# Performance work log

Hardware: AMD Instinct MI355X
Metric: run time of the kernel (lower is better)

## Reference

```python
import jax, jax.numpy as jnp
import numpy as np

B = 256
M = (32, 32, 32)          # size_in modes
N = (32, 32, 32)          # size_out modes
R = (1, 16, 16, 1)        # TT ranks
CORE_SCALE = 0.05


def setup_inputs() -> dict:
    key = jax.random.key(0)
    kx, k0, k1, k2, kb = jax.random.split(key, 5)
    x = jax.random.normal(kx, (B,) + M, dtype=jnp.float32)
    # TT cores: core_i has shape [r_i, n_i, m_i, r_{i+1}]
    core0 = jax.random.normal(k0, (R[0], N[0], M[0], R[1]), dtype=jnp.float32) * CORE_SCALE
    core1 = jax.random.normal(k1, (R[1], N[1], M[1], R[2]), dtype=jnp.float32) * CORE_SCALE
    core2 = jax.random.normal(k2, (R[2], N[2], M[2], R[3]), dtype=jnp.float32) * CORE_SCALE
    bias = jax.random.normal(kb, N, dtype=jnp.float32) * 0.01
    return {"x": x, "core0": core0, "core1": core1, "core2": core2, "bias": bias}


def _tt_matvec(x, cores):
    # y[..., n1..nd] = sum_{m1..md} prod_i core_i[r_i, n_i, m_i, r_{i+1}] * x[..., m1..md]
    d = len(cores)
    batch_shape = x.shape[:-d]
    # z: [B, r, P, m_i, m_{i+1}, ..., m_d]  (P = flattened already-produced n dims)
    z = x.reshape((-1, 1, 1) + x.shape[-d:])
    n_dims = []
    for core in cores:
        r, n, m, s = core.shape
        # contract current input mode m and left rank r; append output mode n
        z = jnp.einsum('rnms,brpm...->bspn...', core, z)
        n_dims.append(n)
        sh = z.shape
        z = z.reshape(sh[:2] + (sh[2] * sh[3],) + sh[4:])  # merge P and n
    return z.reshape(batch_shape + tuple(n_dims))


def reference(x, core0, core1, core2, bias):
    y = _tt_matvec(x, (core0, core1, core2))
    return y + bias
```

## Files before the change

### kernel.cpp

```cpp
#include <hip/hip_runtime.h>


typedef __attribute__((ext_vector_type(8))) short bf16x8;
typedef __attribute__((ext_vector_type(4))) float f32x4;

#define WS_A1   0
#define WS_A0T  262144
#define WS_W2T  278528
#define WS_XT   294912
#define WS_XT_ELEMS 8388608
#define WS_NEED_BYTES ((size_t)(WS_XT + WS_XT_ELEMS) * 2)

__device__ __forceinline__ unsigned short f2bf(float f) {
    union { float f; unsigned int u; } v; v.f = f;
    unsigned int u = v.u;
    u += 0x7fffu + ((u >> 16) & 1u);
    return (unsigned short)(u >> 16);
}

template<bool XT>
__global__ void tt_prep(const float* __restrict__ x,
                        const float* __restrict__ core0,
                        const float* __restrict__ core1,
                        const float* __restrict__ core2,
                        unsigned short* __restrict__ ws)
{
    const int t = threadIdx.x;
    if (XT && blockIdx.x < 8192) {
        __shared__ float tile[32 * 36];
        const int b  = blockIdx.x >> 5;
        const int m2 = blockIdx.x & 31;
        {
            const int m1 = t >> 3, c4 = (t & 7) * 4;
            float4 v = *(const float4*)(x + (size_t)b * 32768 + m1 * 1024 + m2 * 32 + c4);
            *(float4*)&tile[m1 * 36 + c4] = v;
        }
        __syncthreads();
        {
            const int m3 = t >> 3, g = t & 7;
            unsigned short o[4];
            #pragma unroll
            for (int j = 0; j < 4; ++j)
                o[j] = f2bf(tile[(g * 4 + j) * 36 + m3]);
            unsigned short* dst = ws + WS_XT + (size_t)b * 32768 + (m2 * 32 + m3) * 32 + g * 4;
            *(uint2*)dst = *(uint2*)o;
        }
        return;
    }
    const int u = (blockIdx.x - (XT ? 8192 : 0)) * 256 + t;
    unsigned short* A1  = ws + WS_A1;
    unsigned short* A0T = ws + WS_A0T;
    unsigned short* W2T = ws + WS_W2T;
    bf16x8 o;
    if (u < 32768) {
        int e = u * 8;
        int row = e >> 9, col0 = e & 511;
        int n2 = row >> 4, s = row & 15;
        int m2 = col0 >> 4, r0 = col0 & 15;
        const float* src = core1 + n2 * 512 + m2 * 16 + s;
        #pragma unroll
        for (int j = 0; j < 8; ++j) o[j] = (short)f2bf(src[(r0 + j) * 16384]);
        *(bf16x8*)(A1 + e) = o;
    } else if (u < 34816) {
        int e = (u - 32768) * 8;
        int row = e >> 5, m1b = e & 31;
        int n1 = row >> 4, s = row & 15;
        const float* src = core0 + n1 * 512 + m1b * 16 + s;
        #pragma unroll
        for (int j = 0; j < 8; ++j) o[j] = (short)f2bf(src[j * 16]);
        *(bf16x8*)(A0T + e) = o;
    } else if (u < 36864) {
        int e = (u - 34816) * 8;
        int n3 = e >> 9, k20 = e & 511;
        int m3 = k20 >> 4, s0 = k20 & 15;
        const float* src = core2 + n3 * 32 + m3;
        #pragma unroll
        for (int j = 0; j < 8; ++j) o[j] = (short)f2bf(src[(s0 + j) * 1024]);
        *(bf16x8*)(W2T + e) = o;
    }
}

template<bool XT>
__global__ __launch_bounds__(512, 2)
void tt_mfma(const float* __restrict__ x,
             const unsigned short* __restrict__ ws,
             const float* __restrict__ bias,
             float* __restrict__ out)
{
    extern __shared__ char smem[];

    const unsigned short* A1  = ws + WS_A1;
    const unsigned short* A0T = ws + WS_A0T;
    const unsigned short* W2T = ws + WS_W2T;
    const unsigned short* xT  = ws + WS_XT;

    const int t   = threadIdx.x;
    const int l   = t & 63;
    const int w   = t >> 6;
    const int l15 = l & 15;
    const int lg  = l >> 4;

    const int swzid = (blockIdx.x & 7) * 256 + (blockIdx.x >> 3);
    const int bq = swzid >> 5;
    const int n1 = swzid & 31;

    const int swz5 = ((l15 >> 1) & 1) << 5;

    {
        const int lb = w >> 1, ph = w & 1;
        const int b  = bq * 4 + lb;
        char* zb = smem + lb * 32768;
        bf16x8 afrag = *(const bf16x8*)(A0T + n1 * 512 + l15 * 32 + lg * 8);
        if (XT) {
            const unsigned short* xb = xT + (size_t)b * 32768 + lg * 8;
            bf16x8 bfrag[2];
            bfrag[0] = *(const bf16x8*)(xb + (ph * 512 + l15) * 32);
            #pragma unroll
            for (int pti = 0; pti < 32; ++pti) {
                if (pti < 31) {
                    int pn = ph * 512 + (pti + 1) * 16 + l15;
                    bfrag[(pti + 1) & 1] = *(const bf16x8*)(xb + pn * 32);
                }
                int p = ph * 512 + pti * 16 + l15;
                f32x4 c = __builtin_amdgcn_mfma_f32_16x16x32_bf16(
                    afrag, bfrag[pti & 1], (f32x4){0.f, 0.f, 0.f, 0.f}, 0, 0, 0);
                int m2 = p >> 5, m3 = p & 31;
                unsigned short h[4];
                #pragma unroll
                for (int i = 0; i < 4; ++i) h[i] = f2bf(c[i]);
                int off = ((m2 >> 1) << 11) + (m3 << 6) +
                          ((((m2 & 1) << 5) + (lg << 3)) ^ (((m3 >> 1) & 1) << 5));
                *(uint2*)(zb + off) = *(uint2*)h;
            }
        } else {
            const float* xb = x + (size_t)b * 32768 + (lg * 8) * 1024;
            for (int pti = 0; pti < 32; ++pti) {
                int p = ph * 512 + pti * 16 + l15;
                bf16x8 bfrag;
                #pragma unroll
                for (int j = 0; j < 8; ++j) bfrag[j] = (short)f2bf(xb[j * 1024 + p]);
                f32x4 c = __builtin_amdgcn_mfma_f32_16x16x32_bf16(
                    afrag, bfrag, (f32x4){0.f, 0.f, 0.f, 0.f}, 0, 0, 0);
                int m2 = p >> 5, m3 = p & 31;
                unsigned short h[4];
                #pragma unroll
                for (int i = 0; i < 4; ++i) h[i] = f2bf(c[i]);
                int off = ((m2 >> 1) << 11) + (m3 << 6) +
                          ((((m2 & 1) << 5) + (lg << 3)) ^ (((m3 >> 1) & 1) << 5));
                *(uint2*)(zb + off) = *(uint2*)h;
            }
        }
    }
    __syncthreads();

    f32x4 acc[4][8];
    #pragma unroll
    for (int mt = 0; mt < 4; ++mt)
        #pragma unroll
        for (int nt = 0; nt < 8; ++nt)
            acc[mt][nt] = (f32x4){0.f, 0.f, 0.f, 0.f};
    {
        const unsigned short* a1p = A1 + (w * 64 + l15) * 512 + lg * 8;
        const int kofs = (lg << 4) ^ swz5;
        const int rlo = (l15 << 6) + kofs;
        const int rhi = rlo + 1024;

        bf16x8 af[2][4], bf[2][8];
        #pragma unroll
        for (int mt = 0; mt < 4; ++mt)
            af[0][mt] = *(const bf16x8*)(a1p + mt * 8192);
        #pragma unroll
        for (int b4 = 0; b4 < 4; ++b4) {
            char* zb = smem + b4 * 32768;
            bf[0][b4 * 2 + 0] = *(const bf16x8*)(zb + rlo);
            bf[0][b4 * 2 + 1] = *(const bf16x8*)(zb + rhi);
        }
        #pragma unroll
        for (int ks = 0; ks < 16; ++ks) {
            const int cur = ks & 1, nxt = cur ^ 1;
            if (ks < 15) {
                #pragma unroll
                for (int mt = 0; mt < 4; ++mt)
                    af[nxt][mt] = *(const bf16x8*)(a1p + mt * 8192 + (ks + 1) * 32);
                #pragma unroll
                for (int b4 = 0; b4 < 4; ++b4) {
                    char* zb = smem + b4 * 32768 + (ks + 1) * 2048;
                    bf[nxt][b4 * 2 + 0] = *(const bf16x8*)(zb + rlo);
                    bf[nxt][b4 * 2 + 1] = *(const bf16x8*)(zb + rhi);
                }
            }
            __builtin_amdgcn_s_setprio(1);
            #pragma unroll
            for (int mt = 0; mt < 4; ++mt)
                #pragma unroll
                for (int nt = 0; nt < 8; ++nt)
                    acc[mt][nt] = __builtin_amdgcn_mfma_f32_16x16x32_bf16(
                        af[cur][mt], bf[cur][nt], acc[mt][nt], 0, 0, 0);
            __builtin_amdgcn_s_setprio(0);
        }
    }
    __syncthreads();

    {
        #pragma unroll
        for (int mt = 0; mt < 4; ++mt) {
            int n2 = w * 4 + mt;
            int nsw = ((n2 >> 1) & 1) << 5;
            #pragma unroll
            for (int nt = 0; nt < 8; ++nt) {
                char* zb = smem + (nt >> 1) * 32768;
                int m3 = (nt & 1) * 16 + l15;
                unsigned short h[4];
                #pragma unroll
                for (int i = 0; i < 4; ++i) h[i] = f2bf(acc[mt][nt][i]);
                int off = ((m3 >> 1) << 11) + (n2 << 6) +
                          ((((m3 & 1) << 5) + (lg << 3)) ^ nsw);
                *(uint2*)(zb + off) = *(uint2*)h;
            }
        }
    }
    __syncthreads();

    {
        const int lb = w >> 1, n3h = w & 1;
        const int b  = bq * 4 + lb;
        char* zb = smem + lb * 32768;
        f32x4 c[2];
        c[0] = (f32x4){0.f, 0.f, 0.f, 0.f};
        c[1] = (f32x4){0.f, 0.f, 0.f, 0.f};
        const unsigned short* w2p = W2T + (n3h * 16 + l15) * 512 + lg * 8;
        const int kofs = (lg << 4) ^ swz5;
        bf16x8 bfg[2];
        bfg[0] = *(const bf16x8*)(w2p);
        #pragma unroll
        for (int ks = 0; ks < 16; ++ks) {
            if (ks < 15) bfg[(ks + 1) & 1] = *(const bf16x8*)(w2p + (ks + 1) * 32);
            #pragma unroll
            for (int mt = 0; mt < 2; ++mt) {
                int n2 = mt * 16 + l15;
                bf16x8 af = *(const bf16x8*)(zb + ks * 2048 + (n2 << 6) + kofs);
                c[mt] = __builtin_amdgcn_mfma_f32_16x16x32_bf16(af, bfg[ks & 1], c[mt], 0, 0, 0);
            }
        }
        int n3 = n3h * 16 + l15;
        size_t ob = (size_t)b * 32768 + (size_t)n1 * 1024;
        const float* bp2 = bias + n1 * 1024;
        #pragma unroll
        for (int mt = 0; mt < 2; ++mt)
            #pragma unroll
            for (int i = 0; i < 4; ++i) {
                int n2 = mt * 16 + lg * 4 + i;
                out[ob + n2 * 32 + n3] = c[mt][i] + bp2[n2 * 32 + n3];
            }
    }
}

extern "C" void kernel_launch(void* const* d_in, const int* in_sizes, int n_in,
                              void* d_out, int out_size, void* d_ws, size_t ws_size,
                              hipStream_t stream) {
    (void)in_sizes; (void)n_in; (void)out_size;
    const float* x     = (const float*)d_in[0];
    const float* core0 = (const float*)d_in[1];
    const float* core1 = (const float*)d_in[2];
    const float* core2 = (const float*)d_in[3];
    const float* bias  = (const float*)d_in[4];
    float* out = (float*)d_out;
    unsigned short* ws = (unsigned short*)d_ws;

    const int lds_bytes = 4 * 32768;
    if (ws_size >= WS_NEED_BYTES) {
        hipFuncSetAttribute((const void*)tt_mfma<true>,
                            hipFuncAttributeMaxDynamicSharedMemorySize, lds_bytes);
        tt_prep<true><<<8336, 256, 0, stream>>>(x, core0, core1, core2, ws);
        tt_mfma<true><<<2048, 512, lds_bytes, stream>>>(x, ws, bias, out);
    } else {
        hipFuncSetAttribute((const void*)tt_mfma<false>,
                            hipFuncAttributeMaxDynamicSharedMemorySize, lds_bytes);
        tt_prep<false><<<144, 256, 0, stream>>>(x, core0, core1, core2, ws);
        tt_mfma<false><<<2048, 512, lds_bytes, stream>>>(x, ws, bias, out);
    }
}
```

Measured before the change: 229.1 us.

## Halve batches per block to cut LDS and registers for higher occupancy

Each block now handles 2 batch elements instead of 4. That halves LDS use to 64 KB and halves the stage-2 accumulator tile, and the launch bounds now request 4 blocks per CU, with twice as many blocks launched. The explicit double-buffered register prefetch of A1 and the LDS fragments is dropped in favour of per-iteration loads with partial unrolling. The aim is to hide latency through occupancy rather than software pipelining. The trade-off is that each A1 fragment loaded from global memory is reused across fewer batches, so global traffic for A1 rises.

```diff
diff --git a/kernel.cpp b/kernel.cpp
--- a/kernel.cpp
+++ b/kernel.cpp
@@ -81,7 +81,7 @@
 }
 
 template<bool XT>
-__global__ __launch_bounds__(512, 2)
+__global__ __launch_bounds__(512, 4)
 void tt_mfma(const float* __restrict__ x,
              const unsigned short* __restrict__ ws,
              const float* __restrict__ bias,
@@ -100,28 +100,28 @@
     const int l15 = l & 15;
     const int lg  = l >> 4;
 
-    const int swzid = (blockIdx.x & 7) * 256 + (blockIdx.x >> 3);
+    const int swzid = (blockIdx.x & 7) * 512 + (blockIdx.x >> 3);
     const int bq = swzid >> 5;
     const int n1 = swzid & 31;
 
     const int swz5 = ((l15 >> 1) & 1) << 5;
 
     {
-        const int lb = w >> 1, ph = w & 1;
-        const int b  = bq * 4 + lb;
+        const int lb = w >> 2, q = w & 3;
+        const int b  = bq * 2 + lb;
         char* zb = smem + lb * 32768;
         bf16x8 afrag = *(const bf16x8*)(A0T + n1 * 512 + l15 * 32 + lg * 8);
         if (XT) {
             const unsigned short* xb = xT + (size_t)b * 32768 + lg * 8;
             bf16x8 bfrag[2];
-            bfrag[0] = *(const bf16x8*)(xb + (ph * 512 + l15) * 32);
-            #pragma unroll
-            for (int pti = 0; pti < 32; ++pti) {
-                if (pti < 31) {
-                    int pn = ph * 512 + (pti + 1) * 16 + l15;
+            bfrag[0] = *(const bf16x8*)(xb + (q * 256 + l15) * 32);
+            #pragma unroll
+            for (int pti = 0; pti < 16; ++pti) {
+                if (pti < 15) {
+                    int pn = (q * 16 + pti + 1) * 16 + l15;
                     bfrag[(pti + 1) & 1] = *(const bf16x8*)(xb + pn * 32);
                 }
-                int p = ph * 512 + pti * 16 + l15;
+                int p = (q * 16 + pti) * 16 + l15;
                 f32x4 c = __builtin_amdgcn_mfma_f32_16x16x32_bf16(
                     afrag, bfrag[pti & 1], (f32x4){0.f, 0.f, 0.f, 0.f}, 0, 0, 0);
                 int m2 = p >> 5, m3 = p & 31;
@@ -134,8 +134,8 @@
             }
         } else {
             const float* xb = x + (size_t)b * 32768 + (lg * 8) * 1024;
-            for (int pti = 0; pti < 32; ++pti) {
-                int p = ph * 512 + pti * 16 + l15;
+            for (int pti = 0; pti < 16; ++pti) {
+                int p = (q * 16 + pti) * 16 + l15;
                 bf16x8 bfrag;
                 #pragma unroll
                 for (int j = 0; j < 8; ++j) bfrag[j] = (short)f2bf(xb[j * 1024 + p]);
@@ -153,11 +153,11 @@
     }
     __syncthreads();
 
-    f32x4 acc[4][8];
+    f32x4 acc[4][4];
     #pragma unroll
     for (int mt = 0; mt < 4; ++mt)
         #pragma unroll
-        for (int nt = 0; nt < 8; ++nt)
+        for (int nt = 0; nt < 4; ++nt)
             acc[mt][nt] = (f32x4){0.f, 0.f, 0.f, 0.f};
     {
         const unsigned short* a1p = A1 + (w * 64 + l15) * 512 + lg * 8;
@@ -165,37 +165,25 @@
         const int rlo = (l15 << 6) + kofs;
         const int rhi = rlo + 1024;
 
-        bf16x8 af[2][4], bf[2][8];
-        #pragma unroll
-        for (int mt = 0; mt < 4; ++mt)
-            af[0][mt] = *(const bf16x8*)(a1p + mt * 8192);
-        #pragma unroll
-        for (int b4 = 0; b4 < 4; ++b4) {
-            char* zb = smem + b4 * 32768;
-            bf[0][b4 * 2 + 0] = *(const bf16x8*)(zb + rlo);
-            bf[0][b4 * 2 + 1] = *(const bf16x8*)(zb + rhi);
-        }
-        #pragma unroll
+        #pragma unroll 2
         for (int ks = 0; ks < 16; ++ks) {
-            const int cur = ks & 1, nxt = cur ^ 1;
-            if (ks < 15) {
-                #pragma unroll
-                for (int mt = 0; mt < 4; ++mt)
-                    af[nxt][mt] = *(const bf16x8*)(a1p + mt * 8192 + (ks + 1) * 32);
-                #pragma unroll
-                for (int b4 = 0; b4 < 4; ++b4) {
-                    char* zb = smem + b4 * 32768 + (ks + 1) * 2048;
-                    bf[nxt][b4 * 2 + 0] = *(const bf16x8*)(zb + rlo);
-                    bf[nxt][b4 * 2 + 1] = *(const bf16x8*)(zb + rhi);
-                }
+            bf16x8 af[4], bf[4];
+            #pragma unroll
+            for (int mt = 0; mt < 4; ++mt)
+                af[mt] = *(const bf16x8*)(a1p + mt * 8192 + ks * 32);
+            #pragma unroll
+            for (int b2 = 0; b2 < 2; ++b2) {
+                char* zb = smem + b2 * 32768 + ks * 2048;
+                bf[b2 * 2 + 0] = *(const bf16x8*)(zb + rlo);
+                bf[b2 * 2 + 1] = *(const bf16x8*)(zb + rhi);
             }
             __builtin_amdgcn_s_setprio(1);
             #pragma unroll
             for (int mt = 0; mt < 4; ++mt)
                 #pragma unroll
-                for (int nt = 0; nt < 8; ++nt)
+                for (int nt = 0; nt < 4; ++nt)
                     acc[mt][nt] = __builtin_amdgcn_mfma_f32_16x16x32_bf16(
-                        af[cur][mt], bf[cur][nt], acc[mt][nt], 0, 0, 0);
+                        af[mt], bf[nt], acc[mt][nt], 0, 0, 0);
             __builtin_amdgcn_s_setprio(0);
         }
     }
@@ -207,7 +195,7 @@
             int n2 = w * 4 + mt;
             int nsw = ((n2 >> 1) & 1) << 5;
             #pragma unroll
-            for (int nt = 0; nt < 8; ++nt) {
+            for (int nt = 0; nt < 4; ++nt) {
                 char* zb = smem + (nt >> 1) * 32768;
                 int m3 = (nt & 1) * 16 + l15;
                 unsigned short h[4];
@@ -222,36 +210,27 @@
     __syncthreads();
 
     {
-        const int lb = w >> 1, n3h = w & 1;
-        const int b  = bq * 4 + lb;
+        const int lb = w >> 2, n2h = (w >> 1) & 1, n3h = w & 1;
+        const int b  = bq * 2 + lb;
         char* zb = smem + lb * 32768;
-        f32x4 c[2];
-        c[0] = (f32x4){0.f, 0.f, 0.f, 0.f};
-        c[1] = (f32x4){0.f, 0.f, 0.f, 0.f};
+        f32x4 c = (f32x4){0.f, 0.f, 0.f, 0.f};
         const unsigned short* w2p = W2T + (n3h * 16 + l15) * 512 + lg * 8;
         const int kofs = (lg << 4) ^ swz5;
-        bf16x8 bfg[2];
-        bfg[0] = *(const bf16x8*)(w2p);
-        #pragma unroll
+        const int n2row = n2h * 16 + l15;
+        #pragma unroll 2
         for (int ks = 0; ks < 16; ++ks) {
-            if (ks < 15) bfg[(ks + 1) & 1] = *(const bf16x8*)(w2p + (ks + 1) * 32);
-            #pragma unroll
-            for (int mt = 0; mt < 2; ++mt) {
-                int n2 = mt * 16 + l15;
-                bf16x8 af = *(const bf16x8*)(zb + ks * 2048 + (n2 << 6) + kofs);
-                c[mt] = __builtin_amdgcn_mfma_f32_16x16x32_bf16(af, bfg[ks & 1], c[mt], 0, 0, 0);
-            }
+            bf16x8 bfg = *(const bf16x8*)(w2p + ks * 32);
+            bf16x8 af  = *(const bf16x8*)(zb + ks * 2048 + (n2row << 6) + kofs);
+            c = __builtin_amdgcn_mfma_f32_16x16x32_bf16(af, bfg, c, 0, 0, 0);
         }
         int n3 = n3h * 16 + l15;
         size_t ob = (size_t)b * 32768 + (size_t)n1 * 1024;
         const float* bp2 = bias + n1 * 1024;
         #pragma unroll
-        for (int mt = 0; mt < 2; ++mt)
-            #pragma unroll
-            for (int i = 0; i < 4; ++i) {
-                int n2 = mt * 16 + lg * 4 + i;
-                out[ob + n2 * 32 + n3] = c[mt][i] + bp2[n2 * 32 + n3];
-            }
+        for (int i = 0; i < 4; ++i) {
+            int n2 = n2h * 16 + lg * 4 + i;
+            out[ob + n2 * 32 + n3] = c[i] + bp2[n2 * 32 + n3];
+        }
     }
 }
 
@@ -267,16 +246,16 @@
     float* out = (float*)d_out;
     unsigned short* ws = (unsigned short*)d_ws;
 
-    const int lds_bytes = 4 * 32768;
+    const int lds_bytes = 2 * 32768;
     if (ws_size >= WS_NEED_BYTES) {
         hipFuncSetAttribute((const void*)tt_mfma<true>,
                             hipFuncAttributeMaxDynamicSharedMemorySize, lds_bytes);
         tt_prep<true><<<8336, 256, 0, stream>>>(x, core0, core1, core2, ws);
-        tt_mfma<true><<<2048, 512, lds_bytes, stream>>>(x, ws, bias, out);
+        tt_mfma<true><<<4096, 512, lds_bytes, stream>>>(x, ws, bias, out);
     } else {
         hipFuncSetAttribute((const void*)tt_mfma<false>,
                             hipFuncAttributeMaxDynamicSharedMemorySize, lds_bytes);
         tt_prep<false><<<144, 256, 0, stream>>>(x, core0, core1, core2, ws);
-        tt_mfma<false><<<2048, 512, lds_bytes, stream>>>(x, ws, bias, out);
-    }
-}
+        tt_mfma<false><<<4096, 512, lds_bytes, stream>>>(x, ws, bias, out);
+    }
+}
```

Measured after the change: 353.5 us. 54.3% more time.
